# Optimization experiments

Measured on AMD Instinct MI355X. Metric: run time of the kernel, lower is better.

## Reference

```python
import jax, jax.numpy as jnp
import numpy as np
from jax import lax

B, C, L = 8, 512, 4096
G, K = 4, 3
PAD = 1
EPS = 1e-5


def setup_inputs() -> dict:
    key = jax.random.key(0)
    ks = jax.random.split(key, 8)
    inp = {
        "input_feat": jax.random.normal(ks[0], (B, C, L), dtype=jnp.float32),
        "x": jax.random.normal(ks[1], (B, C, L), dtype=jnp.float32),
        # depthwise Conv1d(channels, channels, k=3, pad=1, groups=channels): weight (C,1,K)
        "conv_w": jax.random.normal(ks[2], (C, 1, K), dtype=jnp.float32) * (1.0 / np.sqrt(K)),
        "conv_b": jax.random.normal(ks[3], (C,), dtype=jnp.float32) * 0.02,
        # BatchNorm1d affine params (module maps 'LN' -> BatchNorm1d)
        "bn_gamma": jnp.ones((C,), dtype=jnp.float32),
        "bn_beta": jnp.zeros((C,), dtype=jnp.float32),
        # offset/weight generators: Linear(C -> G*K). Source inits to zero (degenerate);
        # use small random values so the deformable path is exercised.
        "off_w": jax.random.normal(ks[4], (G * K, C), dtype=jnp.float32) * 0.02,
        "off_b": jax.random.normal(ks[5], (G * K,), dtype=jnp.float32) * 0.02,
        "wgt_w": jax.random.normal(ks[6], (G * K, C), dtype=jnp.float32) * 0.02,
        "wgt_b": jax.random.normal(ks[7], (G * K,), dtype=jnp.float32) * 0.02,
    }
    return inp


def _forward(x, conv_w, conv_b, bn_gamma, bn_beta, off_w, off_b, wgt_w, wgt_b):
    Bx, Cx, Lx = x.shape
    gs = Cx // G  # group size along channel axis

    # --- spectral_conv: depthwise conv1d + BatchNorm (batch stats) + exact GELU ---
    y = lax.conv_general_dilated(
        x, conv_w, window_strides=(1,), padding=[(PAD, PAD)],
        dimension_numbers=("NCH", "OIH", "NCH"), feature_group_count=Cx,
    ) + conv_b[None, :, None]
    mean = jnp.mean(y, axis=(0, 2), keepdims=True)
    var = jnp.var(y, axis=(0, 2), keepdims=True)
    y = (y - mean) * lax.rsqrt(var + EPS) * bn_gamma[None, :, None] + bn_beta[None, :, None]
    y = jax.nn.gelu(y, approximate=False)  # torch nn.GELU default is exact erf

    feat = y.transpose(0, 2, 1)  # (B, L, C)
    offsets = (feat @ off_w.T + off_b).reshape(Bx, Lx, G, K)
    weights = jax.nn.softmax((feat @ wgt_w.T + wgt_b).reshape(Bx, Lx, G, K), axis=-1)

    # --- deformable spectral gather + bilinear interp + softmax blend ---
    xg = x.transpose(0, 2, 1).reshape(Bx, Lx, G, gs)  # (B, L, G, gs)
    base = jnp.arange(gs, dtype=x.dtype)
    # sample positions: (B, L, G, K, gs)
    idx = jnp.clip(base[None, None, None, None, :] + offsets[..., None], 0.0, gs - 1)
    fl = jnp.floor(idx)
    frac = idx - fl
    fli = jnp.clip(fl, 0, gs - 1).astype(jnp.int32)
    cei = jnp.clip(jnp.ceil(idx), 0, gs - 1).astype(jnp.int32)

    xe = jnp.broadcast_to(xg[:, :, :, None, :], idx.shape)  # (B, L, G, K, gs)
    x_floor = jnp.take_along_axis(xe, fli, axis=-1)
    x_ceil = jnp.take_along_axis(xe, cei, axis=-1)
    interp = x_floor * (1.0 - frac) + x_ceil * frac  # (B, L, G, K, gs)

    out = jnp.sum(interp * weights[..., None], axis=3)  # (B, L, G, gs)
    return out.reshape(Bx, Lx, Cx).transpose(0, 2, 1)  # (B, C, L)


def reference(input_feat, x, conv_w, conv_b, bn_gamma, bn_beta, off_w, off_b, wgt_w, wgt_b):
    # input_feat is accepted but unused, matching the source forward signature.
    return _forward(x, conv_w, conv_b, bn_gamma, bn_beta, off_w, off_b, wgt_w, wgt_b)
```

## Files before the change

kernel.cpp:

```cpp
#include <hip/hip_runtime.h>
#include <math.h>

#define BB 8
#define CC 512
#define LL 4096
#define GG 4
#define KK 3
#define EPSV 1e-5f

#define TLA 32
#define FTP 520
#define LCH 64
#define XPW 134

#define WB_F32OFF 9216
#define PRO_OFF   17408
#define PRW_OFF   (PRO_OFF + BB * LL * 12)

typedef float  f32x4_t  __attribute__((ext_vector_type(4)));
typedef __bf16 bf16x8_t __attribute__((ext_vector_type(8)));

__device__ __forceinline__ float gelu_tanh(float z) {
    float z2 = z * z;
    float a  = 1.5957691216f * fmaf(0.044715f * z2, z, z);
    return z * __builtin_amdgcn_rcpf(1.f + __expf(-a));
}

__device__ __forceinline__ ushort f32_to_bf16(float f) {
    uint u = __float_as_uint(f);
    return (ushort)((u + 0x7fffu + ((u >> 16) & 1u)) >> 16);
}

__device__ __forceinline__ f32x4_t mfma_bf16(uint4 a, uint4 b, f32x4_t c) {
    return __builtin_amdgcn_mfma_f32_16x16x32_bf16(
        __builtin_bit_cast(bf16x8_t, a), __builtin_bit_cast(bf16x8_t, b), c, 0, 0, 0);
}

__global__ __launch_bounds__(256) void conv_stats_kernel(
    const float* __restrict__ x, const float* __restrict__ conv_w,
    const float* __restrict__ conv_b, float* __restrict__ ws)
{
    const int c = blockIdx.x;
    const int b = blockIdx.y;
    const int t = threadIdx.x;

    const float w0 = conv_w[c * 3 + 0];
    const float w1 = conv_w[c * 3 + 1];
    const float w2 = conv_w[c * 3 + 2];
    const float cb = conv_b[c];
    const float* xr = x + ((size_t)b * CC + c) * LL;

    float s = 0.f, ss = 0.f;
#pragma unroll
    for (int i = 0; i < 4; ++i) {
        const int l0 = 4 * (t + 256 * i);
        float4 q = *reinterpret_cast<const float4*>(xr + l0);
        float lf = __shfl_up(q.w, 1);
        if ((t & 63) == 0) lf = (l0 == 0) ? 0.f : xr[l0 - 1];
        float rt = __shfl_down(q.x, 1);
        if ((t & 63) == 63) rt = (l0 + 4 >= LL) ? 0.f : xr[l0 + 4];
        float y;
        y = fmaf(w0, lf,  fmaf(w1, q.x, fmaf(w2, q.y, cb))); s += y; ss = fmaf(y, y, ss);
        y = fmaf(w0, q.x, fmaf(w1, q.y, fmaf(w2, q.z, cb))); s += y; ss = fmaf(y, y, ss);
        y = fmaf(w0, q.y, fmaf(w1, q.z, fmaf(w2, q.w, cb))); s += y; ss = fmaf(y, y, ss);
        y = fmaf(w0, q.z, fmaf(w1, q.w, fmaf(w2, rt,  cb))); s += y; ss = fmaf(y, y, ss);
    }

#pragma unroll
    for (int d = 32; d > 0; d >>= 1) {
        s  += __shfl_down(s,  d, 64);
        ss += __shfl_down(ss, d, 64);
    }
    __shared__ float ls[4], lss[4];
    const int wid = t >> 6, lane = t & 63;
    if (lane == 0) { ls[wid] = s; lss[wid] = ss; }
    __syncthreads();
    if (t == 0) {
        ws[c * 8 + b]        = ls[0] + ls[1] + ls[2] + ls[3];
        ws[4096 + c * 8 + b] = lss[0] + lss[1] + lss[2] + lss[3];
    }
}

__global__ __launch_bounds__(512) void bn_finalize_kernel(
    const float* __restrict__ bn_gamma, const float* __restrict__ bn_beta,
    const float* __restrict__ off_w, const float* __restrict__ wgt_w,
    float* __restrict__ ws)
{
    const int t = threadIdx.x;
    {
        const int c = t;
        float s = 0.f, ss = 0.f;
#pragma unroll
        for (int b = 0; b < 8; ++b) {
            s  += ws[c * 8 + b];
            ss += ws[4096 + c * 8 + b];
        }
        const float inv  = 1.f / (float)(BB * LL);
        const float mean = s * inv;
        const float var  = ss * inv - mean * mean;
        const float sc   = bn_gamma[c] * rsqrtf(var + EPSV);
        ws[8192 + c] = sc;
        ws[8704 + c] = bn_beta[c] - mean * sc;
    }
    ushort* wb = reinterpret_cast<ushort*>(ws + WB_F32OFF);
    const int o  = t >> 4;
    const int k0 = (t & 15) * 32;
    uint* dst = reinterpret_cast<uint*>(wb + o * CC + k0);
    if (o < 24) {
        const float* src = (o < 12) ? (off_w + o * CC + k0) : (wgt_w + (o - 12) * CC + k0);
#pragma unroll 4
        for (int j = 0; j < 16; ++j) {
            float2 v = *reinterpret_cast<const float2*>(src + 2 * j);
            dst[j] = (uint)f32_to_bf16(v.x) | ((uint)f32_to_bf16(v.y) << 16);
        }
    } else {
#pragma unroll 4
        for (int j = 0; j < 16; ++j) dst[j] = 0u;
    }
}

__global__ __launch_bounds__(512, 8) void proj_coeffs_kernel(
    const float* __restrict__ x,
    const float* __restrict__ conv_w, const float* __restrict__ conv_b,
    const float* __restrict__ off_b,  const float* __restrict__ wgt_b,
    float* __restrict__ ws)
{
    __shared__ ushort ftb[TLA][FTP];
    __shared__ float  pr[TLA][24];

    const int t  = threadIdx.x;
    const int b  = blockIdx.y;
    const int l0 = blockIdx.x * TLA;

    {
        const int ch = t;
        const float* xr = x + ((size_t)b * CC + ch) * LL + l0;
        const float w0 = conv_w[ch*3+0], w1 = conv_w[ch*3+1], w2 = conv_w[ch*3+2];
        const float sc = ws[8192 + ch];
        const float sh = fmaf(conv_b[ch], sc, ws[8704 + ch]);

        float cz = 0.f;
        float cw = (l0 == 0) ? 0.f : xr[-1];
#pragma unroll
        for (int i = 0; i < 8; ++i) {
            float4 q = *reinterpret_cast<const float4*>(xr + 4 * i);
            if (i > 0) {
                float cv = fmaf(w0, cz, fmaf(w1, cw, w2 * q.x));
                ftb[4*i-1][ch] = f32_to_bf16(gelu_tanh(fmaf(sc, cv, sh)));
            }
            float c0 = fmaf(w0, cw,  fmaf(w1, q.x, w2 * q.y));
            ftb[4*i+0][ch] = f32_to_bf16(gelu_tanh(fmaf(sc, c0, sh)));
            float c1 = fmaf(w0, q.x, fmaf(w1, q.y, w2 * q.z));
            ftb[4*i+1][ch] = f32_to_bf16(gelu_tanh(fmaf(sc, c1, sh)));
            float c2 = fmaf(w0, q.y, fmaf(w1, q.z, w2 * q.w));
            ftb[4*i+2][ch] = f32_to_bf16(gelu_tanh(fmaf(sc, c2, sh)));
            cz = q.z; cw = q.w;
        }
        float e2 = (l0 + TLA >= LL) ? 0.f : xr[TLA];
        float cv = fmaf(w0, cz, fmaf(w1, cw, w2 * e2));
        ftb[TLA-1][ch] = f32_to_bf16(gelu_tanh(fmaf(sc, cv, sh)));
    }
    __syncthreads();

    const int wv = t >> 6, lane = t & 63;
    if (wv < 4) {
        const int msub = wv >> 1;
        const int n    = lane & 15;
        const int kb   = (lane >> 4) * 8;
        const ushort* wrow = reinterpret_cast<const ushort*>(ws + WB_F32OFF)
                             + ((wv & 1) * 16 + n) * CC + kb;
        const ushort* arow = &ftb[msub * 16 + n][kb];
        f32x4_t acc = {0.f, 0.f, 0.f, 0.f};
#pragma unroll
        for (int s = 0; s < CC / 32; ++s) {
            uint4 av = *reinterpret_cast<const uint4*>(arow + 32 * s);
            uint4 bv = *reinterpret_cast<const uint4*>(wrow + 32 * s);
            acc = mfma_bf16(av, bv, acc);
        }
        const int o = (wv & 1) * 16 + n;
        if (o < 24) {
            float bias = (o < 12) ? off_b[o] : wgt_b[o - 12];
            const int rb = (lane >> 4) * 4;
#pragma unroll
            for (int i = 0; i < 4; ++i) pr[msub * 16 + rb + i][o] = acc[i] + bias;
        }
    }
    __syncthreads();

    if (t < TLA * 12) {
        const int l  = t / 12;
        const int gk = t - l * 12;
        const int g  = gk / 3;
        const int k  = gk - g * 3;
        float s0 = pr[l][12 + g*3 + 0];
        float s1 = pr[l][12 + g*3 + 1];
        float s2 = pr[l][12 + g*3 + 2];
        float m  = fmaxf(s0, fmaxf(s1, s2));
        float e0 = __expf(s0 - m), e1 = __expf(s1 - m), e2 = __expf(s2 - m);
        float ek = (k == 0) ? e0 : ((k == 1) ? e1 : e2);
        float w  = ek * __builtin_amdgcn_rcpf(e0 + e1 + e2);
        const int base = ((b << 12) + l0) * 12;
        ws[PRO_OFF + base + t] = pr[l][g*3 + k];
        ws[PRW_OFF + base + t] = w;
    }
}

__global__ __launch_bounds__(512, 8) void gather_kernel(
    const float* __restrict__ x, const float* __restrict__ ws,
    float* __restrict__ out)
{
    __shared__ float xpad[LCH][XPW];
    __shared__ float W6[LCH][6];

    const int t  = threadIdx.x;
    const int l0 = blockIdx.x * LCH;
    const int g  = blockIdx.y;
    const int b  = blockIdx.z;
    const int gbase = g << 7;
    const float* xg = x + ((size_t)b * CC + gbase) * LL;

#pragma unroll
    for (int i = 0; i < 4; ++i) {
        const int idx = i * 512 + t;
        const int c   = idx >> 4;
        const int lq4 = idx & 15;
        float4 q = *reinterpret_cast<const float4*>(xg + (size_t)c * LL + l0 + 4 * lq4);
        xpad[4*lq4+0][c+3] = q.x;
        xpad[4*lq4+1][c+3] = q.y;
        xpad[4*lq4+2][c+3] = q.z;
        xpad[4*lq4+3][c+3] = q.w;
    }
    if (t < LCH) {
        const int l = t;
        float xl = xg[l0 + l];
        float xrgt = xg[(size_t)127 * LL + l0 + l];
        xpad[l][0] = xl;  xpad[l][1] = xl;  xpad[l][2] = xl;
        xpad[l][131] = xrgt; xpad[l][132] = xrgt; xpad[l][133] = xrgt;

        const int base = ((b << 12) + l0 + l) * 12 + g * 3;
        float w6_0 = 0.f, w6_1 = 0.f, w6_2 = 0.f, w6_3 = 0.f, w6_4 = 0.f, w6_5 = 0.f;
#pragma unroll
        for (int k = 0; k < KK; ++k) {
            float off = ws[PRO_OFF + base + k];
            float w   = ws[PRW_OFF + base + k];
            float fo  = floorf(off);
            float fr  = off - fo;
            int d = (int)fo + 3;
            d = min(max(d, 0), 4);
            float wa = w * (1.f - fr);
            float wb = w * fr;
            w6_0 += (d == 0) ? wa : 0.f;
            w6_1 += (d == 1) ? wa : 0.f;  w6_1 += (d == 0) ? wb : 0.f;
            w6_2 += (d == 2) ? wa : 0.f;  w6_2 += (d == 1) ? wb : 0.f;
            w6_3 += (d == 3) ? wa : 0.f;  w6_3 += (d == 2) ? wb : 0.f;
            w6_4 += (d == 4) ? wa : 0.f;  w6_4 += (d == 3) ? wb : 0.f;
            w6_5 += (d == 4) ? wb : 0.f;
        }
        W6[l][0] = w6_0; W6[l][1] = w6_1; W6[l][2] = w6_2;
        W6[l][3] = w6_3; W6[l][4] = w6_4; W6[l][5] = w6_5;
    }
    __syncthreads();

    const int c2 = t & 127;
    const int lq = t >> 7;
    float oacc[16];
#pragma unroll
    for (int il = 0; il < 16; ++il) {
        const int l = lq * 16 + il;
        const float* xr = &xpad[l][c2];
        const float* wr = &W6[l][0];
        float a = wr[0] * xr[0];
        a = fmaf(wr[1], xr[1], a);
        a = fmaf(wr[2], xr[2], a);
        a = fmaf(wr[3], xr[3], a);
        a = fmaf(wr[4], xr[4], a);
        a = fmaf(wr[5], xr[5], a);
        oacc[il] = a;
    }
    float* orow = out + ((size_t)b * CC + gbase + c2) * LL + l0 + lq * 16;
#pragma unroll
    for (int i = 0; i < 4; ++i) {
        *reinterpret_cast<float4*>(orow + 4 * i) =
            make_float4(oacc[4*i], oacc[4*i+1], oacc[4*i+2], oacc[4*i+3]);
    }
}

extern "C" void kernel_launch(void* const* d_in, const int* in_sizes, int n_in,
                              void* d_out, int out_size, void* d_ws, size_t ws_size,
                              hipStream_t stream) {
    const float* x      = (const float*)d_in[1];
    const float* conv_w = (const float*)d_in[2];
    const float* conv_b = (const float*)d_in[3];
    const float* bn_g   = (const float*)d_in[4];
    const float* bn_b   = (const float*)d_in[5];
    const float* off_w  = (const float*)d_in[6];
    const float* off_b  = (const float*)d_in[7];
    const float* wgt_w  = (const float*)d_in[8];
    const float* wgt_b  = (const float*)d_in[9];
    float* out = (float*)d_out;
    float* ws  = (float*)d_ws;

    conv_stats_kernel<<<dim3(CC, BB), 256, 0, stream>>>(x, conv_w, conv_b, ws);
    bn_finalize_kernel<<<1, 512, 0, stream>>>(bn_g, bn_b, off_w, wgt_w, ws);
    proj_coeffs_kernel<<<dim3(LL / TLA, BB), 512, 0, stream>>>(
        x, conv_w, conv_b, off_b, wgt_b, ws);
    gather_kernel<<<dim3(LL / LCH, GG, BB), 512, 0, stream>>>(x, ws, out);
}
```

Before: 236.9 us.

## Fuse projection/coefficient and gather kernels into one tile kernel

```diff
diff --git a/kernel.cpp b/kernel.cpp
--- a/kernel.cpp
+++ b/kernel.cpp
@@ -8,14 +8,11 @@
 #define KK 3
 #define EPSV 1e-5f
 
-#define TLA 32
+#define TL 32
 #define FTP 520
-#define LCH 64
-#define XPW 134
+#define XGW 136
 
 #define WB_F32OFF 9216
-#define PRO_OFF   17408
-#define PRW_OFF   (PRO_OFF + BB * LL * 12)
 
 typedef float  f32x4_t  __attribute__((ext_vector_type(4)));
 typedef __bf16 bf16x8_t __attribute__((ext_vector_type(8)));
@@ -29,6 +26,10 @@
 __device__ __forceinline__ ushort f32_to_bf16(float f) {
     uint u = __float_as_uint(f);
     return (ushort)((u + 0x7fffu + ((u >> 16) & 1u)) >> 16);
+}
+
+__device__ __forceinline__ float bf16_to_f32(ushort h) {
+    return __uint_as_float((uint)h << 16);
 }
 
 __device__ __forceinline__ f32x4_t mfma_bf16(uint4 a, uint4 b, f32x4_t c) {
@@ -119,21 +120,27 @@
     }
 }
 
-__global__ __launch_bounds__(512, 8) void proj_coeffs_kernel(
+__global__ __launch_bounds__(512, 4) void mega_kernel(
     const float* __restrict__ x,
     const float* __restrict__ conv_w, const float* __restrict__ conv_b,
     const float* __restrict__ off_b,  const float* __restrict__ wgt_b,
-    float* __restrict__ ws)
+    const float* __restrict__ ws, float* __restrict__ out)
 {
-    __shared__ ushort ftb[TLA][FTP];
-    __shared__ float  pr[TLA][24];
+    __shared__ ushort xt[TL][GG][XGW];
+    __shared__ ushort ftb[TL][FTP];
+    __shared__ float  pr[TL][24];
+    __shared__ float  W6[TL][GG][6];
 
     const int t  = threadIdx.x;
     const int b  = blockIdx.y;
-    const int l0 = blockIdx.x * TLA;
+    const int bx = blockIdx.x;
+    const int ltile = ((bx & 7) << 4) | (bx >> 3);
+    const int l0 = ltile * TL;
 
     {
         const int ch = t;
+        const int g  = ch >> 7;
+        const int j  = ch & 127;
         const float* xr = x + ((size_t)b * CC + ch) * LL + l0;
         const float w0 = conv_w[ch*3+0], w1 = conv_w[ch*3+1], w2 = conv_w[ch*3+2];
         const float sc = ws[8192 + ch];
@@ -144,6 +151,10 @@
 #pragma unroll
         for (int i = 0; i < 8; ++i) {
             float4 q = *reinterpret_cast<const float4*>(xr + 4 * i);
+            xt[4*i+0][g][3+j] = f32_to_bf16(q.x);
+            xt[4*i+1][g][3+j] = f32_to_bf16(q.y);
+            xt[4*i+2][g][3+j] = f32_to_bf16(q.z);
+            xt[4*i+3][g][3+j] = f32_to_bf16(q.w);
             if (i > 0) {
                 float cv = fmaf(w0, cz, fmaf(w1, cw, w2 * q.x));
                 ftb[4*i-1][ch] = f32_to_bf16(gelu_tanh(fmaf(sc, cv, sh)));
@@ -156,9 +167,24 @@
             ftb[4*i+2][ch] = f32_to_bf16(gelu_tanh(fmaf(sc, c2, sh)));
             cz = q.z; cw = q.w;
         }
-        float e2 = (l0 + TLA >= LL) ? 0.f : xr[TLA];
+        float e2 = (l0 + TL >= LL) ? 0.f : xr[TL];
         float cv = fmaf(w0, cz, fmaf(w1, cw, w2 * e2));
-        ftb[TLA-1][ch] = f32_to_bf16(gelu_tanh(fmaf(sc, cv, sh)));
+        ftb[TL-1][ch] = f32_to_bf16(gelu_tanh(fmaf(sc, cv, sh)));
+
+        if (j == 0) {
+#pragma unroll
+            for (int l = 0; l < TL; ++l) {
+                ushort v = xt[l][g][3];
+                xt[l][g][0] = v; xt[l][g][1] = v; xt[l][g][2] = v;
+            }
+        }
+        if (j == 127) {
+#pragma unroll
+            for (int l = 0; l < TL; ++l) {
+                ushort v = xt[l][g][130];
+                xt[l][g][131] = v; xt[l][g][132] = v; xt[l][g][133] = v;
+            }
+        }
     }
     __syncthreads();
 
@@ -187,68 +213,25 @@
     }
     __syncthreads();
 
-    if (t < TLA * 12) {
-        const int l  = t / 12;
-        const int gk = t - l * 12;
-        const int g  = gk / 3;
-        const int k  = gk - g * 3;
+    if (t < TL * GG) {
+        const int l = t >> 2, g = t & 3;
         float s0 = pr[l][12 + g*3 + 0];
         float s1 = pr[l][12 + g*3 + 1];
         float s2 = pr[l][12 + g*3 + 2];
         float m  = fmaxf(s0, fmaxf(s1, s2));
         float e0 = __expf(s0 - m), e1 = __expf(s1 - m), e2 = __expf(s2 - m);
-        float ek = (k == 0) ? e0 : ((k == 1) ? e1 : e2);
-        float w  = ek * __builtin_amdgcn_rcpf(e0 + e1 + e2);
-        const int base = ((b << 12) + l0) * 12;
-        ws[PRO_OFF + base + t] = pr[l][g*3 + k];
-        ws[PRW_OFF + base + t] = w;
-    }
-}
-
-__global__ __launch_bounds__(512, 8) void gather_kernel(
-    const float* __restrict__ x, const float* __restrict__ ws,
-    float* __restrict__ out)
-{
-    __shared__ float xpad[LCH][XPW];
-    __shared__ float W6[LCH][6];
-
-    const int t  = threadIdx.x;
-    const int l0 = blockIdx.x * LCH;
-    const int g  = blockIdx.y;
-    const int b  = blockIdx.z;
-    const int gbase = g << 7;
-    const float* xg = x + ((size_t)b * CC + gbase) * LL;
-
-#pragma unroll
-    for (int i = 0; i < 4; ++i) {
-        const int idx = i * 512 + t;
-        const int c   = idx >> 4;
-        const int lq4 = idx & 15;
-        float4 q = *reinterpret_cast<const float4*>(xg + (size_t)c * LL + l0 + 4 * lq4);
-        xpad[4*lq4+0][c+3] = q.x;
-        xpad[4*lq4+1][c+3] = q.y;
-        xpad[4*lq4+2][c+3] = q.z;
-        xpad[4*lq4+3][c+3] = q.w;
-    }
-    if (t < LCH) {
-        const int l = t;
-        float xl = xg[l0 + l];
-        float xrgt = xg[(size_t)127 * LL + l0 + l];
-        xpad[l][0] = xl;  xpad[l][1] = xl;  xpad[l][2] = xl;
-        xpad[l][131] = xrgt; xpad[l][132] = xrgt; xpad[l][133] = xrgt;
-
-        const int base = ((b << 12) + l0 + l) * 12 + g * 3;
+        float inv = __builtin_amdgcn_rcpf(e0 + e1 + e2);
+        float wks[3] = {e0 * inv, e1 * inv, e2 * inv};
         float w6_0 = 0.f, w6_1 = 0.f, w6_2 = 0.f, w6_3 = 0.f, w6_4 = 0.f, w6_5 = 0.f;
 #pragma unroll
         for (int k = 0; k < KK; ++k) {
-            float off = ws[PRO_OFF + base + k];
-            float w   = ws[PRW_OFF + base + k];
+            float off = pr[l][g*3 + k];
             float fo  = floorf(off);
             float fr  = off - fo;
             int d = (int)fo + 3;
             d = min(max(d, 0), 4);
-            float wa = w * (1.f - fr);
-            float wb = w * fr;
+            float wa = wks[k] * (1.f - fr);
+            float wb = wks[k] * fr;
             w6_0 += (d == 0) ? wa : 0.f;
             w6_1 += (d == 1) ? wa : 0.f;  w6_1 += (d == 0) ? wb : 0.f;
             w6_2 += (d == 2) ? wa : 0.f;  w6_2 += (d == 1) ? wb : 0.f;
@@ -256,32 +239,36 @@
             w6_4 += (d == 4) ? wa : 0.f;  w6_4 += (d == 3) ? wb : 0.f;
             w6_5 += (d == 4) ? wb : 0.f;
         }
-        W6[l][0] = w6_0; W6[l][1] = w6_1; W6[l][2] = w6_2;
-        W6[l][3] = w6_3; W6[l][4] = w6_4; W6[l][5] = w6_5;
-    }
-    __syncthreads();
-
-    const int c2 = t & 127;
-    const int lq = t >> 7;
-    float oacc[16];
-#pragma unroll
-    for (int il = 0; il < 16; ++il) {
-        const int l = lq * 16 + il;
-        const float* xr = &xpad[l][c2];
-        const float* wr = &W6[l][0];
-        float a = wr[0] * xr[0];
-        a = fmaf(wr[1], xr[1], a);
-        a = fmaf(wr[2], xr[2], a);
-        a = fmaf(wr[3], xr[3], a);
-        a = fmaf(wr[4], xr[4], a);
-        a = fmaf(wr[5], xr[5], a);
-        oacc[il] = a;
-    }
-    float* orow = out + ((size_t)b * CC + gbase + c2) * LL + l0 + lq * 16;
-#pragma unroll
-    for (int i = 0; i < 4; ++i) {
-        *reinterpret_cast<float4*>(orow + 4 * i) =
-            make_float4(oacc[4*i], oacc[4*i+1], oacc[4*i+2], oacc[4*i+3]);
+        W6[l][g][0] = w6_0; W6[l][g][1] = w6_1; W6[l][g][2] = w6_2;
+        W6[l][g][3] = w6_3; W6[l][g][4] = w6_4; W6[l][g][5] = w6_5;
+    }
+    __syncthreads();
+
+    {
+        const int ch = t, g = ch >> 7, j = ch & 127;
+        float* orow = out + ((size_t)b * CC + ch) * LL + l0;
+#pragma unroll
+        for (int h = 0; h < 4; ++h) {
+            float acc[8];
+#pragma unroll
+            for (int u = 0; u < 8; ++u) {
+                const int l = h * 8 + u;
+                const ushort* xr2 = &xt[l][g][j];
+                const float*  w6  = &W6[l][g][0];
+                float a = w6[0] * bf16_to_f32(xr2[0]);
+                a = fmaf(w6[1], bf16_to_f32(xr2[1]), a);
+                a = fmaf(w6[2], bf16_to_f32(xr2[2]), a);
+                a = fmaf(w6[3], bf16_to_f32(xr2[3]), a);
+                a = fmaf(w6[4], bf16_to_f32(xr2[4]), a);
+                a = fmaf(w6[5], bf16_to_f32(xr2[5]), a);
+                acc[u] = a;
+            }
+#pragma unroll
+            for (int i = 0; i < 2; ++i) {
+                *reinterpret_cast<float4*>(orow + h * 8 + 4 * i) =
+                    make_float4(acc[4*i], acc[4*i+1], acc[4*i+2], acc[4*i+3]);
+            }
+        }
     }
 }
 
@@ -302,7 +289,6 @@
 
     conv_stats_kernel<<<dim3(CC, BB), 256, 0, stream>>>(x, conv_w, conv_b, ws);
     bn_finalize_kernel<<<1, 512, 0, stream>>>(bn_g, bn_b, off_w, wgt_w, ws);
-    proj_coeffs_kernel<<<dim3(LL / TLA, BB), 512, 0, stream>>>(
-        x, conv_w, conv_b, off_b, wgt_b, ws);
-    gather_kernel<<<dim3(LL / LCH, GG, BB), 512, 0, stream>>>(x, ws, out);
-}
+    mega_kernel<<<dim3(LL / TL, BB), 512, 0, stream>>>(
+        x, conv_w, conv_b, off_b, wgt_b, ws, out);
+}
```

New measurement: 223.4 us. -5.7%, faster.
